# Kernel tuning notes

Measured on AMD Instinct MI355X. Metric: run time of the kernel, lower is better.

The kernel has to match this reference:

```python
import jax, jax.numpy as jnp
import numpy as np
import math

B, T = 64, 2000
RNN_DIM, EMB_DIM, ATT_DIM = 1024, 512, 128
STATIC_CH, STATIC_K = 8, 21
DYN_CH, DYN_K = 8, 21
PRIOR_LEN, ALPHA, BETA = 11, 0.1, 0.9


def _betabinom_pmf(k, n, a, b):
    lg = math.lgamma
    return math.exp(lg(n + 1) - lg(k + 1) - lg(n - k + 1)
                    + lg(k + a) + lg(n - k + b) - lg(n + a + b)
                    - (lg(a) + lg(b) - lg(a + b)))


def setup_inputs() -> dict:
    key = jax.random.key(0)
    ks = jax.random.split(key, 12)
    query = jax.random.normal(ks[0], (B, RNN_DIM), jnp.float32)
    memory = jax.random.normal(ks[1], (B, T, EMB_DIM), jnp.float32)
    a = jax.random.uniform(ks[2], (B, T), jnp.float32)
    alignment_pre = a / jnp.sum(a, axis=1, keepdims=True)  # valid attention distribution
    mask = jnp.zeros((B, T), dtype=bool)
    s = 1.0 / math.sqrt(RNN_DIM)
    W_w = jax.random.uniform(ks[3], (ATT_DIM, RNN_DIM), jnp.float32, -s, s)
    W_b = jax.random.uniform(ks[4], (ATT_DIM,), jnp.float32, -s, s)
    V_w = jax.random.normal(ks[5], (DYN_CH * DYN_K, ATT_DIM), jnp.float32) * 0.05
    F_w = jax.random.normal(ks[6], (STATIC_CH, 1, STATIC_K), jnp.float32) * 0.1
    U_w = jax.random.normal(ks[7], (ATT_DIM, STATIC_CH), jnp.float32) * 0.1
    T_w = jax.random.normal(ks[8], (ATT_DIM, DYN_CH), jnp.float32) * 0.1
    T_b = jax.random.normal(ks[9], (ATT_DIM,), jnp.float32) * 0.05
    v_w = jax.random.normal(ks[10], (1, ATT_DIM), jnp.float32) * 0.1
    P_np = np.array([_betabinom_pmf(k, PRIOR_LEN - 1, ALPHA, BETA) for k in range(PRIOR_LEN)], np.float32)
    P = jnp.asarray(P_np[::-1].copy())  # buffer: flipped beta-binomial prior
    return {"attention_hidden_state": query, "memory": memory, "alignment_pre": alignment_pre,
            "mask": mask, "W_w": W_w, "W_b": W_b, "V_w": V_w, "F_w": F_w,
            "U_w": U_w, "T_w": T_w, "T_b": T_b, "v_w": v_w, "P": P}


def _conv1d(lhs, rhs, pad, groups=1):
    # lhs [N,C,T], rhs [O,C//groups,K]; cross-correlation, matching torch conv1d
    return jax.lax.conv_general_dilated(lhs, rhs, (1,), [pad],
                                        dimension_numbers=("NCH", "OIH", "NCH"),
                                        feature_group_count=groups)


def reference(attention_hidden_state, memory, alignment_pre, mask,
              W_w, W_b, V_w, F_w, U_w, T_w, T_b, v_w, P):
    b, t = alignment_pre.shape
    # log of causal beta-binomial prior: left-pad by prior_length-1, valid conv
    p = _conv1d(alignment_pre[:, None, :], P.reshape(1, 1, -1), (PRIOR_LEN - 1, 0))[:, 0, :]
    p = jnp.log(jnp.clip(p, 1e-6))
    # per-sample dynamic kernels: [B, dyn_ch*K]
    G = jnp.tanh(attention_hidden_state @ W_w.T + W_b) @ V_w.T
    g = _conv1d(alignment_pre[None, :, :], G.reshape(b * DYN_CH, 1, DYN_K),
                ((DYN_K - 1) // 2, (DYN_K - 1) // 2), groups=b)  # [1, B*dyn_ch, T]
    g = g.reshape(b, DYN_CH, t).transpose(0, 2, 1)  # [B, T, dyn_ch]
    # static conv features
    f = _conv1d(alignment_pre[:, None, :], F_w,
                ((STATIC_K - 1) // 2, (STATIC_K - 1) // 2)).transpose(0, 2, 1)  # [B, T, static_ch]
    e = (jnp.tanh(f @ U_w.T + g @ T_w.T + T_b) @ v_w.T)[..., 0] + p  # [B, T]
    e = jnp.where(mask, -jnp.inf, e)
    attention_weights = jax.nn.softmax(e, axis=1)
    attention_context = jnp.einsum("bt,bte->be", attention_weights, memory)
    return attention_context, attention_weights
```

## Files before the change

### kernel.cpp

```cpp
#include <hip/hip_runtime.h>

#define B_   64
#define T_   2000
#define RNN_ 1024
#define EMB_ 512
#define ATT_ 128
#define CH_  8
#define K_   21
#define PL_  11
#define GSZ  168
#define ECHK 128
#define NEC  16
#define CCHK 64
#define NCC  32

typedef float vf4 __attribute__((ext_vector_type(4)));

__device__ __forceinline__ float fast_tanh(float x) {
    float ax = fabsf(x);
    float e  = __expf(2.0f * ax);
    float t  = 1.0f - 2.0f / (e + 1.0f);
    return copysignf(t, x);
}

__global__ __launch_bounds__(256) void k_gen_dyn(
    const float* __restrict__ q, const float* __restrict__ Ww,
    const float* __restrict__ Wb, const float* __restrict__ Vw,
    float* __restrict__ G, float* __restrict__ out_ctx)
{
    __shared__ float sq[RNN_];
    __shared__ float part[256];
    __shared__ float sh[ATT_];
    const int b = blockIdx.x, tid = threadIdx.x;
    for (int i = tid; i < EMB_; i += 256) out_ctx[b * EMB_ + i] = 0.f;
    for (int i = tid; i < RNN_; i += 256) sq[i] = q[b * RNN_ + i];
    __syncthreads();
    {
        const int row = tid & 127, half = tid >> 7;
        const float4* wr = reinterpret_cast<const float4*>(Ww + row * RNN_ + half * (RNN_ / 2));
        const float4* qr = reinterpret_cast<const float4*>(sq + half * (RNN_ / 2));
        float acc = 0.f;
        #pragma unroll 8
        for (int i = 0; i < RNN_ / 8; ++i) {
            float4 w4 = wr[i], q4 = qr[i];
            acc += w4.x * q4.x + w4.y * q4.y + w4.z * q4.z + w4.w * q4.w;
        }
        part[tid] = acc;
    }
    __syncthreads();
    if (tid < ATT_) sh[tid] = fast_tanh(part[tid] + part[tid + 128] + Wb[tid]);
    __syncthreads();
    for (int o = tid; o < GSZ; o += 256) {
        const float4* vr = reinterpret_cast<const float4*>(Vw + o * ATT_);
        const float4* hr = reinterpret_cast<const float4*>(sh);
        float acc = 0.f;
        #pragma unroll 8
        for (int i = 0; i < ATT_ / 4; ++i) {
            float4 v4 = vr[i], h4 = hr[i];
            acc += v4.x * h4.x + v4.y * h4.y + v4.z * h4.z + v4.w * h4.w;
        }
        G[b * GSZ + o] = acc;
    }
}

__global__ __launch_bounds__(256) void k_energy(
    const float* __restrict__ a,  const float* __restrict__ G,
    const float* __restrict__ Fw, const float* __restrict__ Uw,
    const float* __restrict__ Tw, const float* __restrict__ Tb,
    const float* __restrict__ vw, const float* __restrict__ P,
    const unsigned char* __restrict__ mask,
    float* __restrict__ pout, float* __restrict__ mred, float* __restrict__ sred)
{
    __shared__ float sA[ECHK + K_ - 1];
    __shared__ float sFG[K_ * 16];
    __shared__ float sUT[ATT_ * 16];
    __shared__ float sTb[ATT_], sV[ATT_], sPr[PL_];
    __shared__ float sQ[2 * ECHK];
    __shared__ float red[4];
    const int b = blockIdx.x, chunk = blockIdx.y, tid = threadIdx.x;
    const int t0 = chunk * ECHK;
    const int base = t0 - (K_ - 1) / 2;
    const int tloc = tid & (ECHK - 1);
    const int h = tid >> 7;

    for (int j = tid; j < ECHK + K_ - 1; j += 256) {
        int idx = base + j;
        sA[j] = (idx >= 0 && idx < T_) ? a[b * T_ + idx] : 0.f;
    }
    for (int j = tid; j < 2 * GSZ; j += 256) {
        if (j < GSZ) sFG[(j % K_) * 16 + (j / K_)] = Fw[j];
        else { int jj = j - GSZ; sFG[(jj % K_) * 16 + 8 + (jj / K_)] = G[b * GSZ + jj]; }
    }
    for (int j = tid; j < ATT_ * CH_; j += 256) {
        int d = j >> 3, c = j & 7;
        sUT[d * 16 + c]     = Uw[j];
        sUT[d * 16 + 8 + c] = Tw[j];
    }
    if (tid < ATT_) { sTb[tid] = Tb[tid]; sV[tid] = vw[tid]; }
    if (tid < PL_)  sPr[tid] = P[tid];
    __syncthreads();

    float fg[16];
    #pragma unroll
    for (int i = 0; i < 16; ++i) fg[i] = 0.f;
    #pragma unroll
    for (int k = 0; k < K_; ++k) {
        float av = sA[tloc + k];
        const float4* fp = reinterpret_cast<const float4*>(&sFG[k * 16]);
        float4 x0 = fp[0], x1 = fp[1], x2 = fp[2], x3 = fp[3];
        fg[0]  += x0.x * av; fg[1]  += x0.y * av; fg[2]  += x0.z * av; fg[3]  += x0.w * av;
        fg[4]  += x1.x * av; fg[5]  += x1.y * av; fg[6]  += x1.z * av; fg[7]  += x1.w * av;
        fg[8]  += x2.x * av; fg[9]  += x2.y * av; fg[10] += x2.z * av; fg[11] += x2.w * av;
        fg[12] += x3.x * av; fg[13] += x3.y * av; fg[14] += x3.z * av; fg[15] += x3.w * av;
    }

    float accQ = 0.f;
    const int d0 = h * 64;
    #pragma unroll 4
    for (int dd = 0; dd < 64; ++dd) {
        const int d = d0 + dd;
        const float4* up = reinterpret_cast<const float4*>(&sUT[d * 16]);
        float4 u0 = up[0], u1 = up[1], u2 = up[2], u3 = up[3];
        float s0 = u0.x * fg[0]  + u0.y * fg[1]  + u0.z * fg[2]  + u0.w * fg[3];
        float s1 = u1.x * fg[4]  + u1.y * fg[5]  + u1.z * fg[6]  + u1.w * fg[7];
        float s2 = u2.x * fg[8]  + u2.y * fg[9]  + u2.z * fg[10] + u2.w * fg[11];
        float s3 = u3.x * fg[12] + u3.y * fg[13] + u3.z * fg[14] + u3.w * fg[15];
        float s = (sTb[d] + s0) + (s1 + s2) + s3;
        accQ += sV[d] * fast_tanh(s);
    }
    sQ[h * ECHK + tloc] = accQ;
    __syncthreads();

    float e = -1e30f;
    const int t = t0 + tid;
    if (tid < ECHK) {
        const bool valid = (t < T_) && !mask[b * T_ + min(t, T_ - 1)];
        if (valid) {
            float pp = 0.f;
            #pragma unroll
            for (int k = 0; k < PL_; ++k) pp += sPr[k] * sA[tid + k];
            e = sQ[tid] + sQ[ECHK + tid] + __logf(fmaxf(pp, 1e-6f));
        }
    }
    float m = e;
    #pragma unroll
    for (int off = 32; off > 0; off >>= 1) m = fmaxf(m, __shfl_xor(m, off));
    if ((tid & 63) == 0) red[tid >> 6] = m;
    __syncthreads();
    const float Mc = fmaxf(fmaxf(red[0], red[1]), fmaxf(red[2], red[3]));
    __syncthreads();
    float pv = (e > -1e29f) ? __expf(e - Mc) : 0.f;
    if (tid < ECHK && t < T_) pout[b * T_ + t] = pv;
    float ssum = pv;
    #pragma unroll
    for (int off = 32; off > 0; off >>= 1) ssum += __shfl_xor(ssum, off);
    if ((tid & 63) == 0) red[tid >> 6] = ssum;
    __syncthreads();
    if (tid == 0) {
        mred[b * NEC + chunk] = Mc;
        sred[b * NEC + chunk] = red[0] + red[1] + red[2] + red[3];
    }
}

__global__ __launch_bounds__(256, 8) void k_ctx(
    const float* __restrict__ mred, const float* __restrict__ sred,
    const float* __restrict__ mem, float* __restrict__ w,
    float* __restrict__ out)
{
    __shared__ float sw_[CCHK];
    __shared__ vf4 sCtx[2][EMB_ / 4];
    const int b = blockIdx.x, chunk = blockIdx.y, tid = threadIdx.x;
    const int t0 = chunk * CCHK;
    const int nvalid = min(CCHK, T_ - t0);

    const float4* mp = reinterpret_cast<const float4*>(mred + b * NEC);
    const float4* sp = reinterpret_cast<const float4*>(sred + b * NEC);
    float4 m0 = mp[0], m1 = mp[1], m2 = mp[2], m3 = mp[3];
    float M = fmaxf(fmaxf(fmaxf(m0.x, m0.y), fmaxf(m0.z, m0.w)),
             fmaxf(fmaxf(fmaxf(m1.x, m1.y), fmaxf(m1.z, m1.w)),
             fmaxf(fmaxf(fmaxf(m2.x, m2.y), fmaxf(m2.z, m2.w)),
                   fmaxf(fmaxf(m3.x, m3.y), fmaxf(m3.z, m3.w)))));
    float4 s0 = sp[0], s1 = sp[1], s2 = sp[2], s3 = sp[3];
    float S = s0.x * __expf(m0.x - M) + s0.y * __expf(m0.y - M)
            + s0.z * __expf(m0.z - M) + s0.w * __expf(m0.w - M)
            + s1.x * __expf(m1.x - M) + s1.y * __expf(m1.y - M)
            + s1.z * __expf(m1.z - M) + s1.w * __expf(m1.w - M)
            + s2.x * __expf(m2.x - M) + s2.y * __expf(m2.y - M)
            + s2.z * __expf(m2.z - M) + s2.w * __expf(m2.w - M)
            + s3.x * __expf(m3.x - M) + s3.y * __expf(m3.y - M)
            + s3.z * __expf(m3.z - M) + s3.w * __expf(m3.w - M);
    const float scale = __expf(mred[b * NEC + (chunk >> 1)] - M) / S;

    if (tid < CCHK) {
        const int t = t0 + tid;
        float wv = 0.f;
        if (t < T_) {
            wv = w[b * T_ + t] * scale;
            w[b * T_ + t] = wv;
        }
        sw_[tid] = wv;
    }
    __syncthreads();

    const int col = tid & 127, rp = tid >> 7;
    const vf4* m4 = reinterpret_cast<const vf4*>(mem + ((size_t)(b * T_ + t0)) * EMB_);
    vf4 acc = {0.f, 0.f, 0.f, 0.f};
    if (nvalid == CCHK) {
        #pragma unroll 8
        for (int tt = rp; tt < CCHK; tt += 2) {
            float wv = sw_[tt];
            vf4 mvv = m4[(size_t)tt * (EMB_ / 4) + col];
            acc += wv * mvv;
        }
    } else {
        for (int tt = rp; tt < nvalid; tt += 2) {
            float wv = sw_[tt];
            vf4 mvv = m4[(size_t)tt * (EMB_ / 4) + col];
            acc += wv * mvv;
        }
    }
    sCtx[rp][col] = acc;
    __syncthreads();
    if (tid < EMB_ / 4) {
        vf4 r = sCtx[0][tid];
        r += sCtx[1][tid];
        float* op = out + b * EMB_ + tid * 4;
        atomicAdd(op + 0, r.x); atomicAdd(op + 1, r.y);
        atomicAdd(op + 2, r.z); atomicAdd(op + 3, r.w);
    }
}

extern "C" void kernel_launch(void* const* d_in, const int* in_sizes, int n_in,
                              void* d_out, int out_size, void* d_ws, size_t ws_size,
                              hipStream_t stream)
{
    const float* q    = (const float*)d_in[0];
    const float* mem  = (const float*)d_in[1];
    const float* a    = (const float*)d_in[2];
    const unsigned char* mask = (const unsigned char*)d_in[3];
    const float* Ww = (const float*)d_in[4];
    const float* Wb = (const float*)d_in[5];
    const float* Vw = (const float*)d_in[6];
    const float* Fw = (const float*)d_in[7];
    const float* Uw = (const float*)d_in[8];
    const float* Tw = (const float*)d_in[9];
    const float* Tb = (const float*)d_in[10];
    const float* vw = (const float*)d_in[11];
    const float* P  = (const float*)d_in[12];

    float* out_ctx = (float*)d_out;
    float* out_w   = out_ctx + B_ * EMB_;

    float* G    = (float*)d_ws;
    float* mred = G + B_ * GSZ;
    float* sred = mred + B_ * NEC;

    k_gen_dyn<<<B_, 256, 0, stream>>>(q, Ww, Wb, Vw, G, out_ctx);
    k_energy<<<dim3(B_, NEC), 256, 0, stream>>>(a, G, Fw, Uw, Tw, Tb, vw, P,
                                                mask, out_w, mred, sred);
    k_ctx<<<dim3(B_, NCC), 256, 0, stream>>>(mred, sred, mem, out_w, out_ctx);
}
```

Measured before the change: 94.22 us.

## Split context reduction over embedding columns instead of time to remove atomics

```diff
diff --git a/kernel.cpp b/kernel.cpp
--- a/kernel.cpp
+++ b/kernel.cpp
@@ -11,8 +11,9 @@
 #define GSZ  168
 #define ECHK 128
 #define NEC  16
-#define CCHK 64
-#define NCC  32
+#define NCS  16
+#define CPS  32
+#define WSEG 125
 
 typedef float vf4 __attribute__((ext_vector_type(4)));
 
@@ -26,13 +27,12 @@
 __global__ __launch_bounds__(256) void k_gen_dyn(
     const float* __restrict__ q, const float* __restrict__ Ww,
     const float* __restrict__ Wb, const float* __restrict__ Vw,
-    float* __restrict__ G, float* __restrict__ out_ctx)
+    float* __restrict__ G)
 {
     __shared__ float sq[RNN_];
     __shared__ float part[256];
     __shared__ float sh[ATT_];
     const int b = blockIdx.x, tid = threadIdx.x;
-    for (int i = tid; i < EMB_; i += 256) out_ctx[b * EMB_ + i] = 0.f;
     for (int i = tid; i < RNN_; i += 256) sq[i] = q[b * RNN_ + i];
     __syncthreads();
     {
@@ -69,7 +69,7 @@
     const float* __restrict__ Tw, const float* __restrict__ Tb,
     const float* __restrict__ vw, const float* __restrict__ P,
     const unsigned char* __restrict__ mask,
-    float* __restrict__ pout, float* __restrict__ mred, float* __restrict__ sred)
+    float* __restrict__ pws, float* __restrict__ mred, float* __restrict__ sred)
 {
     __shared__ float sA[ECHK + K_ - 1];
     __shared__ float sFG[K_ * 16];
@@ -150,7 +150,7 @@
     const float Mc = fmaxf(fmaxf(red[0], red[1]), fmaxf(red[2], red[3]));
     __syncthreads();
     float pv = (e > -1e29f) ? __expf(e - Mc) : 0.f;
-    if (tid < ECHK && t < T_) pout[b * T_ + t] = pv;
+    if (tid < ECHK && t < T_) pws[b * T_ + t] = pv;
     float ssum = pv;
     #pragma unroll
     for (int off = 32; off > 0; off >>= 1) ssum += __shfl_xor(ssum, off);
@@ -162,71 +162,59 @@
     }
 }
 
-__global__ __launch_bounds__(256, 8) void k_ctx(
+__global__ __launch_bounds__(256) void k_ctx(
     const float* __restrict__ mred, const float* __restrict__ sred,
-    const float* __restrict__ mem, float* __restrict__ w,
-    float* __restrict__ out)
-{
-    __shared__ float sw_[CCHK];
-    __shared__ vf4 sCtx[2][EMB_ / 4];
-    const int b = blockIdx.x, chunk = blockIdx.y, tid = threadIdx.x;
-    const int t0 = chunk * CCHK;
-    const int nvalid = min(CCHK, T_ - t0);
-
-    const float4* mp = reinterpret_cast<const float4*>(mred + b * NEC);
-    const float4* sp = reinterpret_cast<const float4*>(sred + b * NEC);
-    float4 m0 = mp[0], m1 = mp[1], m2 = mp[2], m3 = mp[3];
-    float M = fmaxf(fmaxf(fmaxf(m0.x, m0.y), fmaxf(m0.z, m0.w)),
-             fmaxf(fmaxf(fmaxf(m1.x, m1.y), fmaxf(m1.z, m1.w)),
-             fmaxf(fmaxf(fmaxf(m2.x, m2.y), fmaxf(m2.z, m2.w)),
-                   fmaxf(fmaxf(m3.x, m3.y), fmaxf(m3.z, m3.w)))));
-    float4 s0 = sp[0], s1 = sp[1], s2 = sp[2], s3 = sp[3];
-    float S = s0.x * __expf(m0.x - M) + s0.y * __expf(m0.y - M)
-            + s0.z * __expf(m0.z - M) + s0.w * __expf(m0.w - M)
-            + s1.x * __expf(m1.x - M) + s1.y * __expf(m1.y - M)
-            + s1.z * __expf(m1.z - M) + s1.w * __expf(m1.w - M)
-            + s2.x * __expf(m2.x - M) + s2.y * __expf(m2.y - M)
-            + s2.z * __expf(m2.z - M) + s2.w * __expf(m2.w - M)
-            + s3.x * __expf(m3.x - M) + s3.y * __expf(m3.y - M)
-            + s3.z * __expf(m3.z - M) + s3.w * __expf(m3.w - M);
-    const float scale = __expf(mred[b * NEC + (chunk >> 1)] - M) / S;
-
-    if (tid < CCHK) {
-        const int t = t0 + tid;
-        float wv = 0.f;
-        if (t < T_) {
-            wv = w[b * T_ + t] * scale;
-            w[b * T_ + t] = wv;
-        }
-        sw_[tid] = wv;
-    }
-    __syncthreads();
-
-    const int col = tid & 127, rp = tid >> 7;
-    const vf4* m4 = reinterpret_cast<const vf4*>(mem + ((size_t)(b * T_ + t0)) * EMB_);
+    const float* __restrict__ pws, const float* __restrict__ mem,
+    float* __restrict__ wout, float* __restrict__ out)
+{
+    __shared__ float sAl[NEC];
+    __shared__ float sw_[T_];
+    __shared__ vf4 sPart[32][8];
+    const int b = blockIdx.x, cs = blockIdx.y, tid = threadIdx.x;
+
+    if (tid < NEC) {
+        float M = -1e30f;
+        #pragma unroll
+        for (int i = 0; i < NEC; ++i) M = fmaxf(M, mred[b * NEC + i]);
+        float S = 0.f;
+        #pragma unroll
+        for (int i = 0; i < NEC; ++i) S += sred[b * NEC + i] * __expf(mred[b * NEC + i] - M);
+        sAl[tid] = __expf(mred[b * NEC + tid] - M) / S;
+    }
+    __syncthreads();
+    for (int j = tid; j < T_; j += 256) sw_[j] = pws[b * T_ + j] * sAl[j >> 7];
+    __syncthreads();
+    if (tid < WSEG) {
+        const int t = cs * WSEG + tid;
+        wout[b * T_ + t] = sw_[t];
+    }
+
+    const int lane = tid & 7, rgrp = tid >> 3;
+    const float* basep = mem + (size_t)b * T_ * EMB_ + cs * CPS + lane * 4;
     vf4 acc = {0.f, 0.f, 0.f, 0.f};
-    if (nvalid == CCHK) {
-        #pragma unroll 8
-        for (int tt = rp; tt < CCHK; tt += 2) {
-            float wv = sw_[tt];
-            vf4 mvv = m4[(size_t)tt * (EMB_ / 4) + col];
-            acc += wv * mvv;
-        }
-    } else {
-        for (int tt = rp; tt < nvalid; tt += 2) {
-            float wv = sw_[tt];
-            vf4 mvv = m4[(size_t)tt * (EMB_ / 4) + col];
-            acc += wv * mvv;
-        }
-    }
-    sCtx[rp][col] = acc;
-    __syncthreads();
-    if (tid < EMB_ / 4) {
-        vf4 r = sCtx[0][tid];
-        r += sCtx[1][tid];
-        float* op = out + b * EMB_ + tid * 4;
-        atomicAdd(op + 0, r.x); atomicAdd(op + 1, r.y);
-        atomicAdd(op + 2, r.z); atomicAdd(op + 3, r.w);
+    #pragma unroll 8
+    for (int i = 0; i < 62; ++i) {
+        const int t = rgrp + i * 32;
+        vf4 mv = *reinterpret_cast<const vf4*>(basep + (size_t)t * EMB_);
+        acc += sw_[t] * mv;
+    }
+    if (rgrp < 16) {
+        const int t = rgrp + 1984;
+        vf4 mv = *reinterpret_cast<const vf4*>(basep + (size_t)t * EMB_);
+        acc += sw_[t] * mv;
+    }
+    sPart[rgrp][lane] = acc;
+    __syncthreads();
+    if (tid < 64) {
+        const int l = tid & 7, qg = tid >> 3;
+        vf4 r = sPart[qg][l] + sPart[qg + 8][l] + sPart[qg + 16][l] + sPart[qg + 24][l];
+        sPart[qg][l] = r;
+    }
+    __syncthreads();
+    if (tid < 8) {
+        vf4 r = sPart[0][tid] + sPart[1][tid] + sPart[2][tid] + sPart[3][tid]
+              + sPart[4][tid] + sPart[5][tid] + sPart[6][tid] + sPart[7][tid];
+        *reinterpret_cast<vf4*>(out + b * EMB_ + cs * CPS + tid * 4) = r;
     }
 }
 
@@ -254,9 +242,10 @@
     float* G    = (float*)d_ws;
     float* mred = G + B_ * GSZ;
     float* sred = mred + B_ * NEC;
-
-    k_gen_dyn<<<B_, 256, 0, stream>>>(q, Ww, Wb, Vw, G, out_ctx);
+    float* pws  = sred + B_ * NEC;
+
+    k_gen_dyn<<<B_, 256, 0, stream>>>(q, Ww, Wb, Vw, G);
     k_energy<<<dim3(B_, NEC), 256, 0, stream>>>(a, G, Fw, Uw, Tw, Tb, vw, P,
-                                                mask, out_w, mred, sred);
-    k_ctx<<<dim3(B_, NCC), 256, 0, stream>>>(mred, sred, mem, out_w, out_ctx);
-}
+                                                mask, pws, mred, sred);
+    k_ctx<<<dim3(B_, NCS), 256, 0, stream>>>(mred, sred, pws, mem, out_w, out_ctx);
+}
```

New measurement: 97.60 us. 1.04x slower.

## Drop softmax max pass and retile context kernel into exact 40-step chunks

Applied to the files above, without the earlier changes.

```diff
diff --git a/kernel.cpp b/kernel.cpp
--- a/kernel.cpp
+++ b/kernel.cpp
@@ -11,8 +11,8 @@
 #define GSZ  168
 #define ECHK 128
 #define NEC  16
-#define CCHK 64
-#define NCC  32
+#define CCHK 40
+#define NCC  50
 
 typedef float vf4 __attribute__((ext_vector_type(4)));
 
@@ -69,7 +69,7 @@
     const float* __restrict__ Tw, const float* __restrict__ Tb,
     const float* __restrict__ vw, const float* __restrict__ P,
     const unsigned char* __restrict__ mask,
-    float* __restrict__ pout, float* __restrict__ mred, float* __restrict__ sred)
+    float* __restrict__ pws, float* __restrict__ sred)
 {
     __shared__ float sA[ECHK + K_ - 1];
     __shared__ float sFG[K_ * 16];
@@ -79,12 +79,11 @@
     __shared__ float red[4];
     const int b = blockIdx.x, chunk = blockIdx.y, tid = threadIdx.x;
     const int t0 = chunk * ECHK;
-    const int base = t0 - (K_ - 1) / 2;
     const int tloc = tid & (ECHK - 1);
     const int h = tid >> 7;
 
     for (int j = tid; j < ECHK + K_ - 1; j += 256) {
-        int idx = base + j;
+        int idx = t0 - 10 + j;
         sA[j] = (idx >= 0 && idx < T_) ? a[b * T_ + idx] : 0.f;
     }
     for (int j = tid; j < 2 * GSZ; j += 256) {
@@ -131,97 +130,64 @@
     sQ[h * ECHK + tloc] = accQ;
     __syncthreads();
 
-    float e = -1e30f;
+    float pv = 0.f;
     const int t = t0 + tid;
     if (tid < ECHK) {
-        const bool valid = (t < T_) && !mask[b * T_ + min(t, T_ - 1)];
-        if (valid) {
+        if (!mask[b * T_ + min(t, T_ - 1)] && t < T_) {
             float pp = 0.f;
             #pragma unroll
             for (int k = 0; k < PL_; ++k) pp += sPr[k] * sA[tid + k];
-            e = sQ[tid] + sQ[ECHK + tid] + __logf(fmaxf(pp, 1e-6f));
+            float e = sQ[tid] + sQ[ECHK + tid] + __logf(fmaxf(pp, 1e-6f));
+            pv = __expf(e);
         }
-    }
-    float m = e;
-    #pragma unroll
-    for (int off = 32; off > 0; off >>= 1) m = fmaxf(m, __shfl_xor(m, off));
-    if ((tid & 63) == 0) red[tid >> 6] = m;
-    __syncthreads();
-    const float Mc = fmaxf(fmaxf(red[0], red[1]), fmaxf(red[2], red[3]));
-    __syncthreads();
-    float pv = (e > -1e29f) ? __expf(e - Mc) : 0.f;
-    if (tid < ECHK && t < T_) pout[b * T_ + t] = pv;
+        if (t < T_) pws[b * T_ + t] = pv;
+    }
     float ssum = pv;
     #pragma unroll
     for (int off = 32; off > 0; off >>= 1) ssum += __shfl_xor(ssum, off);
     if ((tid & 63) == 0) red[tid >> 6] = ssum;
     __syncthreads();
-    if (tid == 0) {
-        mred[b * NEC + chunk] = Mc;
-        sred[b * NEC + chunk] = red[0] + red[1] + red[2] + red[3];
-    }
-}
-
-__global__ __launch_bounds__(256, 8) void k_ctx(
-    const float* __restrict__ mred, const float* __restrict__ sred,
-    const float* __restrict__ mem, float* __restrict__ w,
+    if (tid == 0) sred[b * NEC + chunk] = red[0] + red[1] + red[2] + red[3];
+}
+
+__global__ __launch_bounds__(256, 4) void k_ctx(
+    const float* __restrict__ sred, const float* __restrict__ pws,
+    const float* __restrict__ mem, float* __restrict__ wout,
     float* __restrict__ out)
 {
     __shared__ float sw_[CCHK];
     __shared__ vf4 sCtx[2][EMB_ / 4];
     const int b = blockIdx.x, chunk = blockIdx.y, tid = threadIdx.x;
     const int t0 = chunk * CCHK;
-    const int nvalid = min(CCHK, T_ - t0);
-
-    const float4* mp = reinterpret_cast<const float4*>(mred + b * NEC);
+    const int col = tid & 127, rp = tid >> 7;
+    const float* basep = mem + ((size_t)(b * T_ + t0)) * EMB_ + col * 4;
+
     const float4* sp = reinterpret_cast<const float4*>(sred + b * NEC);
-    float4 m0 = mp[0], m1 = mp[1], m2 = mp[2], m3 = mp[3];
-    float M = fmaxf(fmaxf(fmaxf(m0.x, m0.y), fmaxf(m0.z, m0.w)),
-             fmaxf(fmaxf(fmaxf(m1.x, m1.y), fmaxf(m1.z, m1.w)),
-             fmaxf(fmaxf(fmaxf(m2.x, m2.y), fmaxf(m2.z, m2.w)),
-                   fmaxf(fmaxf(m3.x, m3.y), fmaxf(m3.z, m3.w)))));
     float4 s0 = sp[0], s1 = sp[1], s2 = sp[2], s3 = sp[3];
-    float S = s0.x * __expf(m0.x - M) + s0.y * __expf(m0.y - M)
-            + s0.z * __expf(m0.z - M) + s0.w * __expf(m0.w - M)
-            + s1.x * __expf(m1.x - M) + s1.y * __expf(m1.y - M)
-            + s1.z * __expf(m1.z - M) + s1.w * __expf(m1.w - M)
-            + s2.x * __expf(m2.x - M) + s2.y * __expf(m2.y - M)
-            + s2.z * __expf(m2.z - M) + s2.w * __expf(m2.w - M)
-            + s3.x * __expf(m3.x - M) + s3.y * __expf(m3.y - M)
-            + s3.z * __expf(m3.z - M) + s3.w * __expf(m3.w - M);
-    const float scale = __expf(mred[b * NEC + (chunk >> 1)] - M) / S;
+    float S = ((s0.x + s0.y) + (s0.z + s0.w)) + ((s1.x + s1.y) + (s1.z + s1.w))
+            + ((s2.x + s2.y) + (s2.z + s2.w)) + ((s3.x + s3.y) + (s3.z + s3.w));
+    const float inv = 1.0f / S;
 
     if (tid < CCHK) {
-        const int t = t0 + tid;
-        float wv = 0.f;
-        if (t < T_) {
-            wv = w[b * T_ + t] * scale;
-            w[b * T_ + t] = wv;
-        }
+        float wv = pws[b * T_ + t0 + tid] * inv;
         sw_[tid] = wv;
-    }
-    __syncthreads();
-
-    const int col = tid & 127, rp = tid >> 7;
-    const vf4* m4 = reinterpret_cast<const vf4*>(mem + ((size_t)(b * T_ + t0)) * EMB_);
-    vf4 acc = {0.f, 0.f, 0.f, 0.f};
-    if (nvalid == CCHK) {
-        #pragma unroll 8
-        for (int tt = rp; tt < CCHK; tt += 2) {
-            float wv = sw_[tt];
-            vf4 mvv = m4[(size_t)tt * (EMB_ / 4) + col];
-            acc += wv * mvv;
-        }
-    } else {
-        for (int tt = rp; tt < nvalid; tt += 2) {
-            float wv = sw_[tt];
-            vf4 mvv = m4[(size_t)tt * (EMB_ / 4) + col];
-            acc += wv * mvv;
-        }
-    }
-    sCtx[rp][col] = acc;
-    __syncthreads();
-    if (tid < EMB_ / 4) {
+        wout[b * T_ + t0 + tid] = wv;
+    }
+    __syncthreads();
+
+    vf4 acc0 = {0.f, 0.f, 0.f, 0.f}, acc1 = {0.f, 0.f, 0.f, 0.f};
+    #pragma unroll
+    for (int i = 0; i < CCHK / 4; ++i) {
+        const int r0 = rp + i * 4;
+        const int r1 = rp + i * 4 + 2;
+        vf4 m0 = *reinterpret_cast<const vf4*>(basep + (size_t)r0 * EMB_);
+        vf4 m1 = *reinterpret_cast<const vf4*>(basep + (size_t)r1 * EMB_);
+        acc0 += sw_[r0] * m0;
+        acc1 += sw_[r1] * m1;
+    }
+    sCtx[rp][col] = acc0 + acc1;
+    __syncthreads();
+    if (tid < 128) {
         vf4 r = sCtx[0][tid];
         r += sCtx[1][tid];
         float* op = out + b * EMB_ + tid * 4;
@@ -252,11 +218,11 @@
     float* out_w   = out_ctx + B_ * EMB_;
 
     float* G    = (float*)d_ws;
-    float* mred = G + B_ * GSZ;
-    float* sred = mred + B_ * NEC;
+    float* sred = G + B_ * GSZ;
+    float* pws  = sred + B_ * NEC;
 
     k_gen_dyn<<<B_, 256, 0, stream>>>(q, Ww, Wb, Vw, G, out_ctx);
     k_energy<<<dim3(B_, NEC), 256, 0, stream>>>(a, G, Fw, Uw, Tw, Tb, vw, P,
-                                                mask, out_w, mred, sred);
-    k_ctx<<<dim3(B_, NCC), 256, 0, stream>>>(mred, sred, mem, out_w, out_ctx);
-}
+                                                mask, pws, sred);
+    k_ctx<<<dim3(B_, NCC), 256, 0, stream>>>(sred, pws, mem, out_w, out_ctx);
+}
```

After: 101.0 us. 1.07x slower.
